# Kernel tuning notes

Measured on AMD Instinct MI355X. Metric: run time of the kernel, lower is better.

The kernel has to match this reference:

```python
import jax, jax.numpy as jnp
import numpy as np

B, C, NC, N, K = 16, 64, 12500, 50000, 8  # batch, channels, cliques, fine nodes, clique size


def setup_inputs() -> dict:
    key = jax.random.key(0)
    k1, k2 = jax.random.split(key)
    inputs = jax.random.normal(k1, (B, C * NC), dtype=jnp.float32)
    # flattened subgraph membership: entry m says clique clique_ids[m] contains node node_ids[m]
    node_ids = jax.random.randint(k2, (NC * K,), 0, N, dtype=jnp.int64)
    clique_ids = jnp.repeat(jnp.arange(NC, dtype=jnp.int64), K)
    return {"inputs": inputs, "node_ids": node_ids, "clique_ids": clique_ids,
            "nodes": N, "n_channels": C}


def reference(inputs, node_ids, clique_ids, nodes, n_channels):
    batch, units = inputs.shape
    n_cliques = units // n_channels
    # [B, C, n_cliques] pooled features (row-major reshape, same as tf.reshape)
    pooled = inputs.reshape(batch, n_channels, n_cliques)
    # gather pooled feature of each membership entry: [B, C, M]
    updates = pooled[:, :, clique_ids]
    # scatter-add into fine-node buffer (duplicates accumulate, like tensor_scatter_nd_add)
    unpool = jnp.zeros((batch, n_channels, nodes), dtype=inputs.dtype)
    unpool = unpool.at[:, :, node_ids].add(updates)
    return unpool.reshape(batch, nodes * n_channels)
```

## Files before the change

kernel.cpp:

```cpp
#include <hip/hip_runtime.h>

#define NCLIQ  12500
#define NODES  50000
#define NEDGE  100000
#define NGRP   64
#define ELLW   16

#define FILL_BLOCKS   ((NEDGE + 255) / 256)
#define COL4          (NCLIQ / 4)
#define PACK_BLOCKS_X ((COL4 + 255) / 256)
#define PACK_BLOCKS   (PACK_BLOCKS_X * NGRP)

#define NODEB 64
#define NBLK  ((NODES + NODEB - 1) / NODEB)

typedef float f32x4 __attribute__((ext_vector_type(4)));


__global__ __launch_bounds__(256) void zero_counts(int4* __restrict__ counts4) {
    int t = blockIdx.x * 256 + threadIdx.x;
    if (t < NODES / 4) counts4[t] = make_int4(0, 0, 0, 0);
}


__global__ __launch_bounds__(256) void fill_pack(const int* __restrict__ node_ids,
                                                 const int* __restrict__ clique_ids,
                                                 int* __restrict__ counts,
                                                 unsigned short* __restrict__ ell16,
                                                 const float* __restrict__ in,
                                                 float* __restrict__ inP) {
    int b   = blockIdx.x;
    int tid = threadIdx.x;
    if (b < FILL_BLOCKS) {
        int e = b * 256 + tid;
        if (e < NEDGE) {
            int n   = node_ids[e];
            int pos = atomicAdd(&counts[n], 1);
            if (pos < ELLW) ell16[(size_t)n * ELLW + pos] = (unsigned short)clique_ids[e];
        }
    } else {
        int pb = b - FILL_BLOCKS;
        int g  = pb / PACK_BLOCKS_X;
        int c4 = (pb % PACK_BLOCKS_X) * 256 + tid;
        if (c4 < COL4) {
            f32x4 v[16];
            #pragma unroll
            for (int j = 0; j < 16; ++j)
                v[j] = *reinterpret_cast<const f32x4*>(
                    in + (size_t)(g * 16 + j) * NCLIQ + 4 * c4);
            #pragma unroll
            for (int ci = 0; ci < 4; ++ci) {
                f32x4* line = reinterpret_cast<f32x4*>(
                    inP + ((size_t)g * NCLIQ + 4 * c4 + ci) * 16);
                #pragma unroll
                for (int q = 0; q < 4; ++q) {
                    f32x4 t = { v[4 * q + 0][ci], v[4 * q + 1][ci],
                                v[4 * q + 2][ci], v[4 * q + 3][ci] };
                    line[q] = t;
                }
            }
        }
    }
}


__global__ __launch_bounds__(256) void gather_ell(const float* __restrict__ inP,
                                                  const int* __restrict__ deg,
                                                  const unsigned short* __restrict__ ell16,
                                                  float* __restrict__ out) {
    __shared__ float lds[2][NODEB][17];
    int b     = blockIdx.x;
    int k     = b & 7;
    int r     = b >> 3;
    int nb    = r % NBLK;
    int pp    = r / NBLK;
    int gA    = pp * 16 + k;
    int gB    = gA + 8;
    int tid   = threadIdx.x;
    int s     = tid >> 2;
    int q     = tid & 3;
    int n     = nb * NODEB + s;

    float4 aA = make_float4(0.f, 0.f, 0.f, 0.f);
    float4 aB = make_float4(0.f, 0.f, 0.f, 0.f);
    if (n < NODES) {
        int d = deg[n];
        const uint4 e = *reinterpret_cast<const uint4*>(ell16 + (size_t)n * ELLW);
        unsigned cs[8] = { e.x & 0xFFFFu, e.x >> 16, e.y & 0xFFFFu, e.y >> 16,
                           e.z & 0xFFFFu, e.z >> 16, e.w & 0xFFFFu, e.w >> 16 };
        const float* __restrict__ baseA = inP + (size_t)gA * NCLIQ * 16 + q * 4;
        const float* __restrict__ baseB = inP + (size_t)gB * NCLIQ * 16 + q * 4;
        #pragma unroll
        for (int i = 0; i < 8; ++i) {
            if (i < d) {
                size_t off = (size_t)cs[i] * 16;
                const float4 pA = *reinterpret_cast<const float4*>(baseA + off);
                const float4 pB = *reinterpret_cast<const float4*>(baseB + off);
                aA.x += pA.x; aA.y += pA.y; aA.z += pA.z; aA.w += pA.w;
                aB.x += pB.x; aB.y += pB.y; aB.z += pB.z; aB.w += pB.w;
            }
        }
        if (d > 8) {
            for (int i = 8; i < d && i < ELLW; ++i) {
                size_t off = (size_t)ell16[(size_t)n * ELLW + i] * 16;
                const float4 pA = *reinterpret_cast<const float4*>(baseA + off);
                const float4 pB = *reinterpret_cast<const float4*>(baseB + off);
                aA.x += pA.x; aA.y += pA.y; aA.z += pA.z; aA.w += pA.w;
                aB.x += pB.x; aB.y += pB.y; aB.z += pB.z; aB.w += pB.w;
            }
        }
    }
    lds[0][s][q * 4 + 0] = aA.x;  lds[0][s][q * 4 + 1] = aA.y;
    lds[0][s][q * 4 + 2] = aA.z;  lds[0][s][q * 4 + 3] = aA.w;
    lds[1][s][q * 4 + 0] = aB.x;  lds[1][s][q * 4 + 1] = aB.y;
    lds[1][s][q * 4 + 2] = aB.z;  lds[1][s][q * 4 + 3] = aB.w;
    __syncthreads();

    int p  = tid >> 4;
    int i4 = (tid & 15) * 4;
    int n0 = nb * NODEB + i4;
    if (n0 + 3 < NODES) {
        f32x4 oA = { lds[0][i4][p], lds[0][i4 + 1][p], lds[0][i4 + 2][p], lds[0][i4 + 3][p] };
        f32x4 oB = { lds[1][i4][p], lds[1][i4 + 1][p], lds[1][i4 + 2][p], lds[1][i4 + 3][p] };
        __builtin_nontemporal_store(oA,
            reinterpret_cast<f32x4*>(out + (size_t)(gA * 16 + p) * NODES + n0));
        __builtin_nontemporal_store(oB,
            reinterpret_cast<f32x4*>(out + (size_t)(gB * 16 + p) * NODES + n0));
    }
}


extern "C" void kernel_launch(void* const* d_in, const int* in_sizes, int n_in,
                              void* d_out, int out_size, void* d_ws, size_t ws_size,
                              hipStream_t stream) {
    const float* in         = (const float*)d_in[0];
    const int*   node_ids   = (const int*)d_in[1];
    const int*   clique_ids = (const int*)d_in[2];
    float*       out        = (float*)d_out;

    int*            counts = (int*)d_ws;
    unsigned short* ell16  = (unsigned short*)(counts + NODES);
    float*          inP    = (float*)((char*)d_ws + 200000 + 1600000);

    zero_counts<<<(NODES / 4 + 255) / 256, 256, 0, stream>>>((int4*)counts);
    fill_pack<<<FILL_BLOCKS + PACK_BLOCKS, 256, 0, stream>>>(node_ids, clique_ids,
                                                             counts, ell16, in, inP);
    gather_ell<<<(NGRP / 2) * NBLK, 256, 0, stream>>>(inP, counts, ell16, out);
}
```

Baseline: 94.28 us.

## Loop over channel-group pairs inside gather blocks, reusing ELL indices

Each gather block now handles four channel-group pairs in an in-kernel loop instead of one, so the grid shrinks by four. The degree and packed ELL index row are loaded once per block and reused across all iterations. The LDS transpose buffer is double-buffered by iteration parity and re-padded to reduce bank conflicts, so only one barrier per iteration is needed. The trade-off is fewer blocks in flight, which leaves less parallelism to hide the latency of the random gathers.

```diff
diff --git a/kernel.cpp b/kernel.cpp
--- a/kernel.cpp
+++ b/kernel.cpp
@@ -13,8 +13,10 @@
 
 #define NODEB 64
 #define NBLK  ((NODES + NODEB - 1) / NODEB)
+#define LPAD  21
 
-typedef float f32x4 __attribute__((ext_vector_type(4)));
+typedef float    f32x4 __attribute__((ext_vector_type(4)));
+typedef unsigned u32x4 __attribute__((ext_vector_type(4)));
 
 
 __global__ __launch_bounds__(256) void zero_counts(int4* __restrict__ counts4) {
@@ -68,64 +70,78 @@
                                                   const int* __restrict__ deg,
                                                   const unsigned short* __restrict__ ell16,
                                                   float* __restrict__ out) {
-    __shared__ float lds[2][NODEB][17];
-    int b     = blockIdx.x;
-    int k     = b & 7;
-    int r     = b >> 3;
-    int nb    = r % NBLK;
-    int pp    = r / NBLK;
-    int gA    = pp * 16 + k;
-    int gB    = gA + 8;
-    int tid   = threadIdx.x;
-    int s     = tid >> 2;
-    int q     = tid & 3;
-    int n     = nb * NODEB + s;
+    __shared__ float lds[2][2][NODEB][LPAD];
+    int b   = blockIdx.x;
+    int k   = b & 7;
+    int nb  = b >> 3;
+    int tid = threadIdx.x;
+    int s   = tid >> 2;
+    int q   = tid & 3;
+    int n   = nb * NODEB + s;
 
-    float4 aA = make_float4(0.f, 0.f, 0.f, 0.f);
-    float4 aB = make_float4(0.f, 0.f, 0.f, 0.f);
+    int d = 0;
+    unsigned cs[8];
+    #pragma unroll
+    for (int i = 0; i < 8; ++i) cs[i] = 0;
     if (n < NODES) {
-        int d = deg[n];
-        const uint4 e = *reinterpret_cast<const uint4*>(ell16 + (size_t)n * ELLW);
-        unsigned cs[8] = { e.x & 0xFFFFu, e.x >> 16, e.y & 0xFFFFu, e.y >> 16,
-                           e.z & 0xFFFFu, e.z >> 16, e.w & 0xFFFFu, e.w >> 16 };
-        const float* __restrict__ baseA = inP + (size_t)gA * NCLIQ * 16 + q * 4;
-        const float* __restrict__ baseB = inP + (size_t)gB * NCLIQ * 16 + q * 4;
-        #pragma unroll
-        for (int i = 0; i < 8; ++i) {
-            if (i < d) {
-                size_t off = (size_t)cs[i] * 16;
-                const float4 pA = *reinterpret_cast<const float4*>(baseA + off);
-                const float4 pB = *reinterpret_cast<const float4*>(baseB + off);
-                aA.x += pA.x; aA.y += pA.y; aA.z += pA.z; aA.w += pA.w;
-                aB.x += pB.x; aB.y += pB.y; aB.z += pB.z; aB.w += pB.w;
-            }
-        }
-        if (d > 8) {
-            for (int i = 8; i < d && i < ELLW; ++i) {
-                size_t off = (size_t)ell16[(size_t)n * ELLW + i] * 16;
-                const float4 pA = *reinterpret_cast<const float4*>(baseA + off);
-                const float4 pB = *reinterpret_cast<const float4*>(baseB + off);
-                aA.x += pA.x; aA.y += pA.y; aA.z += pA.z; aA.w += pA.w;
-                aB.x += pB.x; aB.y += pB.y; aB.z += pB.z; aB.w += pB.w;
-            }
-        }
+        d = deg[n];
+        const u32x4 e = *reinterpret_cast<const u32x4*>(ell16 + (size_t)n * ELLW);
+        cs[0] = e.x & 0xFFFFu; cs[1] = e.x >> 16;
+        cs[2] = e.y & 0xFFFFu; cs[3] = e.y >> 16;
+        cs[4] = e.z & 0xFFFFu; cs[5] = e.z >> 16;
+        cs[6] = e.w & 0xFFFFu; cs[7] = e.w >> 16;
     }
-    lds[0][s][q * 4 + 0] = aA.x;  lds[0][s][q * 4 + 1] = aA.y;
-    lds[0][s][q * 4 + 2] = aA.z;  lds[0][s][q * 4 + 3] = aA.w;
-    lds[1][s][q * 4 + 0] = aB.x;  lds[1][s][q * 4 + 1] = aB.y;
-    lds[1][s][q * 4 + 2] = aB.z;  lds[1][s][q * 4 + 3] = aB.w;
-    __syncthreads();
 
     int p  = tid >> 4;
     int i4 = (tid & 15) * 4;
     int n0 = nb * NODEB + i4;
-    if (n0 + 3 < NODES) {
-        f32x4 oA = { lds[0][i4][p], lds[0][i4 + 1][p], lds[0][i4 + 2][p], lds[0][i4 + 3][p] };
-        f32x4 oB = { lds[1][i4][p], lds[1][i4 + 1][p], lds[1][i4 + 2][p], lds[1][i4 + 3][p] };
-        __builtin_nontemporal_store(oA,
-            reinterpret_cast<f32x4*>(out + (size_t)(gA * 16 + p) * NODES + n0));
-        __builtin_nontemporal_store(oB,
-            reinterpret_cast<f32x4*>(out + (size_t)(gB * 16 + p) * NODES + n0));
+
+    for (int pp = 0; pp < 4; ++pp) {
+        int gA  = pp * 16 + k;
+        int gB  = gA + 8;
+        int par = pp & 1;
+
+        float4 aA = make_float4(0.f, 0.f, 0.f, 0.f);
+        float4 aB = make_float4(0.f, 0.f, 0.f, 0.f);
+        if (n < NODES) {
+            const float* __restrict__ baseA = inP + (size_t)gA * NCLIQ * 16 + q * 4;
+            const float* __restrict__ baseB = inP + (size_t)gB * NCLIQ * 16 + q * 4;
+            #pragma unroll
+            for (int i = 0; i < 8; ++i) {
+                if (i < d) {
+                    size_t off = (size_t)cs[i] * 16;
+                    const float4 pA = *reinterpret_cast<const float4*>(baseA + off);
+                    const float4 pB = *reinterpret_cast<const float4*>(baseB + off);
+                    aA.x += pA.x; aA.y += pA.y; aA.z += pA.z; aA.w += pA.w;
+                    aB.x += pB.x; aB.y += pB.y; aB.z += pB.z; aB.w += pB.w;
+                }
+            }
+            if (d > 8) {
+                for (int i = 8; i < d && i < ELLW; ++i) {
+                    size_t off = (size_t)ell16[(size_t)n * ELLW + i] * 16;
+                    const float4 pA = *reinterpret_cast<const float4*>(baseA + off);
+                    const float4 pB = *reinterpret_cast<const float4*>(baseB + off);
+                    aA.x += pA.x; aA.y += pA.y; aA.z += pA.z; aA.w += pA.w;
+                    aB.x += pB.x; aB.y += pB.y; aB.z += pB.z; aB.w += pB.w;
+                }
+            }
+        }
+        lds[par][0][s][q * 4 + 0] = aA.x;  lds[par][0][s][q * 4 + 1] = aA.y;
+        lds[par][0][s][q * 4 + 2] = aA.z;  lds[par][0][s][q * 4 + 3] = aA.w;
+        lds[par][1][s][q * 4 + 0] = aB.x;  lds[par][1][s][q * 4 + 1] = aB.y;
+        lds[par][1][s][q * 4 + 2] = aB.z;  lds[par][1][s][q * 4 + 3] = aB.w;
+        __syncthreads();
+
+        if (n0 + 3 < NODES) {
+            f32x4 oA = { lds[par][0][i4][p],     lds[par][0][i4 + 1][p],
+                         lds[par][0][i4 + 2][p], lds[par][0][i4 + 3][p] };
+            f32x4 oB = { lds[par][1][i4][p],     lds[par][1][i4 + 1][p],
+                         lds[par][1][i4 + 2][p], lds[par][1][i4 + 3][p] };
+            __builtin_nontemporal_store(oA,
+                reinterpret_cast<f32x4*>(out + (size_t)(gA * 16 + p) * NODES + n0));
+            __builtin_nontemporal_store(oB,
+                reinterpret_cast<f32x4*>(out + (size_t)(gB * 16 + p) * NODES + n0));
+        }
     }
 }
 
@@ -145,5 +161,5 @@
     zero_counts<<<(NODES / 4 + 255) / 256, 256, 0, stream>>>((int4*)counts);
     fill_pack<<<FILL_BLOCKS + PACK_BLOCKS, 256, 0, stream>>>(node_ids, clique_ids,
                                                              counts, ell16, in, inP);
-    gather_ell<<<(NGRP / 2) * NBLK, 256, 0, stream>>>(inP, counts, ell16, out);
+    gather_ell<<<8 * NBLK, 256, 0, stream>>>(inP, counts, ell16, out);
 }
```

Result: slower. 110.6 us (+17.3%).
